# Optimization experiments

Hardware: AMD Instinct MI355X
Metric: run time of the kernel (lower is better)

The kernel has to match this reference:

```python
import jax, jax.numpy as jnp
import numpy as np

B, G, P = 4096, 31, 8
C = P * (P + 1) // 2  # 36 pairwise-with-replacement combinations


def setup_inputs() -> dict:
    key = jax.random.key(0)
    k1, k2 = jax.random.split(key)
    param_tensor = jax.random.normal(k1, (B, G, G, P), dtype=jnp.float32)
    integral_coeffs = jax.random.normal(k2, (G, G, C), dtype=jnp.float32)
    return {"param_tensor": param_tensor, "integral_coeffs": integral_coeffs}


def reference(param_tensor, integral_coeffs):
    # torch.combinations(param, 2, with_replacement=True).prod(-1) over last dim
    # == param[ii] * param[jj] for upper-triangular-with-diagonal index pairs.
    P_ = param_tensor.shape[-1]
    ii, jj = np.triu_indices(P_)  # same ordering as torch.combinations with_replacement
    pairs = param_tensor[..., ii] * param_tensor[..., jj]  # [B, G, G, C]
    # weight by per-cell coeffs, sum over pair dim and over both grid dims -> [B]
    return jnp.einsum('bghc,ghc->b', pairs, integral_coeffs)
```

## Files before the change

### kernel.cpp

```cpp
#include <hip/hip_runtime.h>

#define B_  4096
#define G_  31
#define GG_ 961
#define P_  8
#define C_  36
#define R_  8

__global__ void zero_kernel(float* out, int n) {
    int i = blockIdx.x * blockDim.x + threadIdx.x;
    if (i < n) out[i] = 0.0f;
}

__global__ __launch_bounds__(256, 4)
void quadform_kernel(const float* __restrict__ param,
                     const float* __restrict__ coef,
                     float* __restrict__ out) {
    const int lane    = threadIdx.x & 63;
    const int wv      = threadIdx.x >> 6;
    const int gh_tile = blockIdx.x * 4 + wv;
    const int gh      = gh_tile * 64 + lane;
    const bool valid  = gh < GG_;
    const int  ghc    = valid ? gh : (GG_ - 1);

    float cf[C_];
    {
        const float4* cp = reinterpret_cast<const float4*>(coef) + (size_t)ghc * (C_ / 4);
        #pragma unroll
        for (int q = 0; q < C_ / 4; ++q) {
            float4 v = cp[q];
            cf[4*q+0] = v.x; cf[4*q+1] = v.y; cf[4*q+2] = v.z; cf[4*q+3] = v.w;
        }
    }
    if (!valid) {
        #pragma unroll
        for (int c = 0; c < C_; ++c) cf[c] = 0.0f;
    }

    const int b0 = blockIdx.y * R_;
    const float4* pb = reinterpret_cast<const float4*>(param);
    const size_t base = ((size_t)b0 * GG_ + ghc) * 2;
    const size_t bstep = (size_t)GG_ * 2;

    float4 qa[4][2], qb[4][2];
    #pragma unroll
    for (int r = 0; r < 4; ++r) {
        qa[r][0] = pb[base + (size_t)r * bstep];
        qa[r][1] = pb[base + (size_t)r * bstep + 1];
    }
    #pragma unroll
    for (int r = 0; r < 4; ++r) {
        qb[r][0] = pb[base + (size_t)(r + 4) * bstep];
        qb[r][1] = pb[base + (size_t)(r + 4) * bstep + 1];
    }

    float s[R_];
    #pragma unroll
    for (int h = 0; h < 2; ++h) {
        #pragma unroll
        for (int r = 0; r < 4; ++r) {
            float4 p0 = h ? qb[r][0] : qa[r][0];
            float4 p1 = h ? qb[r][1] : qa[r][1];
            const float pv[P_] = {p0.x, p0.y, p0.z, p0.w, p1.x, p1.y, p1.z, p1.w};
            float acc = 0.0f;
            int c = 0;
            #pragma unroll
            for (int i = 0; i < P_; ++i) {
                #pragma unroll
                for (int j = i; j < P_; ++j) {
                    acc = fmaf(cf[c] * pv[i], pv[j], acc);
                    ++c;
                }
            }
            s[h * 4 + r] = acc;
        }
    }

    #pragma unroll
    for (int off = 32; off; off >>= 1) {
        #pragma unroll
        for (int r = 0; r < R_; ++r) s[r] += __shfl_xor(s[r], off, 64);
    }

    if (lane == 0) {
        #pragma unroll
        for (int r = 0; r < R_; ++r) atomicAdd(&out[b0 + r], s[r]);
    }
}

extern "C" void kernel_launch(void* const* d_in, const int* in_sizes, int n_in,
                              void* d_out, int out_size, void* d_ws, size_t ws_size,
                              hipStream_t stream) {
    const float* param = (const float*)d_in[0];
    const float* coef  = (const float*)d_in[1];
    float* out = (float*)d_out;

    zero_kernel<<<(B_ + 255) / 256, 256, 0, stream>>>(out, B_);

    dim3 grid(4, B_ / R_);
    quadform_kernel<<<grid, 256, 0, stream>>>(param, coef, out);
}
```

Baseline: 186.7 us.

## Double-buffer param loads over 16 rows, factor quadratic form, reduce atomics via LDS

```diff
diff --git a/kernel.cpp b/kernel.cpp
--- a/kernel.cpp
+++ b/kernel.cpp
@@ -5,14 +5,17 @@
 #define GG_ 961
 #define P_  8
 #define C_  36
-#define R_  8
+#define R_  16
+#define CH_ 4
+
+typedef float floatx4 __attribute__((ext_vector_type(4)));
 
 __global__ void zero_kernel(float* out, int n) {
     int i = blockIdx.x * blockDim.x + threadIdx.x;
     if (i < n) out[i] = 0.0f;
 }
 
-__global__ __launch_bounds__(256, 4)
+__global__ __launch_bounds__(256, 3)
 void quadform_kernel(const float* __restrict__ param,
                      const float* __restrict__ coef,
                      float* __restrict__ out) {
@@ -23,12 +26,32 @@
     const bool valid  = gh < GG_;
     const int  ghc    = valid ? gh : (GG_ - 1);
 
+    const int b0 = blockIdx.y * R_;
+    const floatx4* pb = reinterpret_cast<const floatx4*>(param);
+    const size_t base  = ((size_t)b0 * GG_ + ghc) * 2;
+    const size_t bstep = (size_t)GG_ * 2;
+
+    floatx4 qA[CH_][2], qB[CH_][2];
+
+#define LOADC(Q, CHK)                                                          \
+    {                                                                          \
+        _Pragma("unroll")                                                      \
+        for (int r = 0; r < CH_; ++r) {                                        \
+            const floatx4* p_ = pb + base + (size_t)((CHK) * CH_ + r) * bstep; \
+            Q[r][0] = __builtin_nontemporal_load(p_);                          \
+            Q[r][1] = __builtin_nontemporal_load(p_ + 1);                      \
+        }                                                                      \
+    }
+
+    LOADC(qA, 0);
+    LOADC(qB, 1);
+
     float cf[C_];
     {
-        const float4* cp = reinterpret_cast<const float4*>(coef) + (size_t)ghc * (C_ / 4);
+        const floatx4* cp = reinterpret_cast<const floatx4*>(coef) + (size_t)ghc * (C_ / 4);
         #pragma unroll
         for (int q = 0; q < C_ / 4; ++q) {
-            float4 v = cp[q];
+            floatx4 v = cp[q];
             cf[4*q+0] = v.x; cf[4*q+1] = v.y; cf[4*q+2] = v.z; cf[4*q+3] = v.w;
         }
     }
@@ -37,44 +60,33 @@
         for (int c = 0; c < C_; ++c) cf[c] = 0.0f;
     }
 
-    const int b0 = blockIdx.y * R_;
-    const float4* pb = reinterpret_cast<const float4*>(param);
-    const size_t base = ((size_t)b0 * GG_ + ghc) * 2;
-    const size_t bstep = (size_t)GG_ * 2;
+    float s[R_];
 
-    float4 qa[4][2], qb[4][2];
-    #pragma unroll
-    for (int r = 0; r < 4; ++r) {
-        qa[r][0] = pb[base + (size_t)r * bstep];
-        qa[r][1] = pb[base + (size_t)r * bstep + 1];
-    }
-    #pragma unroll
-    for (int r = 0; r < 4; ++r) {
-        qb[r][0] = pb[base + (size_t)(r + 4) * bstep];
-        qb[r][1] = pb[base + (size_t)(r + 4) * bstep + 1];
+#define DO_CHUNK(Q, S0)                                                        \
+    {                                                                          \
+        _Pragma("unroll")                                                      \
+        for (int r = 0; r < CH_; ++r) {                                        \
+            const float pv[P_] = {Q[r][0].x, Q[r][0].y, Q[r][0].z, Q[r][0].w,  \
+                                  Q[r][1].x, Q[r][1].y, Q[r][1].z, Q[r][1].w}; \
+            float acc = 0.0f;                                                  \
+            int c = 0;                                                         \
+            _Pragma("unroll")                                                  \
+            for (int i = 0; i < P_; ++i) {                                     \
+                float t = 0.0f;                                                \
+                _Pragma("unroll")                                              \
+                for (int j = i; j < P_; ++j) { t = fmaf(cf[c], pv[j], t); ++c; } \
+                acc = fmaf(pv[i], t, acc);                                     \
+            }                                                                  \
+            s[(S0) + r] = acc;                                                 \
+        }                                                                      \
     }
 
-    float s[R_];
-    #pragma unroll
-    for (int h = 0; h < 2; ++h) {
-        #pragma unroll
-        for (int r = 0; r < 4; ++r) {
-            float4 p0 = h ? qb[r][0] : qa[r][0];
-            float4 p1 = h ? qb[r][1] : qa[r][1];
-            const float pv[P_] = {p0.x, p0.y, p0.z, p0.w, p1.x, p1.y, p1.z, p1.w};
-            float acc = 0.0f;
-            int c = 0;
-            #pragma unroll
-            for (int i = 0; i < P_; ++i) {
-                #pragma unroll
-                for (int j = i; j < P_; ++j) {
-                    acc = fmaf(cf[c] * pv[i], pv[j], acc);
-                    ++c;
-                }
-            }
-            s[h * 4 + r] = acc;
-        }
-    }
+    DO_CHUNK(qA, 0);
+    LOADC(qA, 2);
+    DO_CHUNK(qB, 4);
+    LOADC(qB, 3);
+    DO_CHUNK(qA, 8);
+    DO_CHUNK(qB, 12);
 
     #pragma unroll
     for (int off = 32; off; off >>= 1) {
@@ -82,9 +94,16 @@
         for (int r = 0; r < R_; ++r) s[r] += __shfl_xor(s[r], off, 64);
     }
 
+    __shared__ float red[4][R_];
     if (lane == 0) {
         #pragma unroll
-        for (int r = 0; r < R_; ++r) atomicAdd(&out[b0 + r], s[r]);
+        for (int r = 0; r < R_; ++r) red[wv][r] = s[r];
+    }
+    __syncthreads();
+    if (threadIdx.x < R_) {
+        const int r = threadIdx.x;
+        float v = red[0][r] + red[1][r] + red[2][r] + red[3][r];
+        atomicAdd(&out[b0 + r], v);
     }
 }
 
```

Result: faster. 176.4 us (median of 2 runs) (-5.5%).
